# Kernel tuning notes

Hardware: AMD Instinct MI355X
Metric: run time of the kernel (lower is better)

Reference implementation:

```python
import jax, jax.numpy as jnp
import numpy as np
from jax import lax

B, SEQ, C, H, W, OUT, K = 64, 32, 16, 128, 256, 10, 2  # batch, timestamps, channels, hidden, width, classes, substeps/interval


def setup_inputs() -> dict:
    key = jax.random.key(0)
    ks = jax.random.split(key, 16)
    p = lambda k, shape, fan_in: (jax.random.normal(k, shape, dtype=jnp.float32) / np.sqrt(fan_in))
    coeff = lambda k: jax.random.normal(k, (B, SEQ - 1, C), dtype=jnp.float32)
    return {
        'ts': jnp.arange(SEQ, dtype=jnp.float32),
        'coeff_d': coeff(ks[0]), 'coeff_c': coeff(ks[1]), 'coeff_b': coeff(ks[2]), 'coeff_a': coeff(ks[3]),
        # initial MLP: in_size -> width -> width -> hidden (relu)
        'iw0': p(ks[4], (W, C), C), 'ib0': jnp.zeros((W,), jnp.float32),
        'iw1': p(ks[5], (W, W), W), 'ib1': jnp.zeros((W,), jnp.float32),
        'iw2': p(ks[6], (H, W), W), 'ib2': jnp.zeros((H,), jnp.float32),
        # vector-field MLP: hidden -> width -> width -> hidden*in_size (softplus, tanh final)
        'fw0': p(ks[7], (W, H), H), 'fb0': jnp.zeros((W,), jnp.float32),
        'fw1': p(ks[8], (W, W), W), 'fb1': jnp.zeros((W,), jnp.float32),
        'fw2': p(ks[9], (H * C, W), W), 'fb2': jnp.zeros((H * C,), jnp.float32),
        # readout linear: hidden -> out
        'lw': p(ks[10], (OUT, H), H), 'lb': jnp.zeros((OUT,), jnp.float32),
    }


def _forward(ts, coeff_d, coeff_c, coeff_b, coeff_a, iw0, ib0, iw1, ib1, iw2, ib2,
             fw0, fb0, fw1, fb1, fw2, fb2, lw, lb):
    nb, ni, c = coeff_a.shape
    h_dim = iw2.shape[0]

    def init_mlp(x):  # [B,C] -> [B,H]
        h = jax.nn.relu(x @ iw0.T + ib0)
        h = jax.nn.relu(h @ iw1.T + ib1)
        return h @ iw2.T + ib2

    def vf(y):  # [B,H] -> [B,H,C]
        h = jax.nn.softplus(y @ fw0.T + fb0)
        h = jax.nn.softplus(h @ fw1.T + fb1)
        return jnp.tanh(h @ fw2.T + fb2).reshape(nb, h_dim, c)

    def dxdt(frac, i):  # derivative of cubic interpolation on interval i: 3d f^2 + 2c f + b
        return (3.0 * coeff_d[:, i] * frac + 2.0 * coeff_c[:, i]) * frac + coeff_b[:, i]

    def f(frac, i, y):  # ControlTerm.to_ode: dy/dt = vf(y) @ dX/dt
        return jnp.einsum('bhc,bc->bh', vf(y), dxdt(frac, i))

    dts = jnp.diff(ts)
    hsub = dts / K
    idx = jnp.repeat(jnp.arange(ni), K)                                # interval index per substep
    hs = jnp.repeat(hsub, K)                                           # substep size
    fr0 = jnp.tile(jnp.arange(K, dtype=ts.dtype), ni) * hs             # offset within interval at substep start

    def step(y, xs):  # one fixed-size Tsit5 step (Tsitouras 2011 tableau)
        t0, h, i = xs
        k1 = f(t0, i, y)
        k2 = f(t0 + 0.161 * h, i, y + h * (0.161 * k1))
        k3 = f(t0 + 0.327 * h, i, y + h * (-0.008480655492356989 * k1 + 0.335480655492357 * k2))
        k4 = f(t0 + 0.9 * h, i, y + h * (2.8971530571054935 * k1 - 6.359448489975075 * k2 + 4.3622954328695815 * k3))
        k5 = f(t0 + 0.9800255409045097 * h, i, y + h * (5.325864828439257 * k1 - 11.748883564062828 * k2 + 7.4955393428898365 * k3 - 0.09249506636175525 * k4))
        k6 = f(t0 + h, i, y + h * (5.86145544294642 * k1 - 12.92096931784711 * k2 + 8.159367898576159 * k3 - 0.071584973281401 * k4 - 0.028269050394068383 * k5))
        y_new = y + h * (0.09646076681806523 * k1 + 0.01 * k2 + 0.4798896504144996 * k3 + 1.379008574103742 * k4 - 3.290069515436081 * k5 + 2.324710524099774 * k6)
        return y_new, None

    y0 = init_mlp(coeff_a[:, 0])  # X(ts[0]) = a-coefficient at frac=0
    yT, _ = lax.scan(step, y0, (fr0, hs, idx))
    return jax.nn.log_softmax(yT @ lw.T + lb, axis=-1)  # out_size != 1 -> log_softmax


def reference(ts, coeff_d, coeff_c, coeff_b, coeff_a, iw0, ib0, iw1, ib1, iw2, ib2,
              fw0, fb0, fw1, fb1, fw2, fb2, lw, lb):
    return _forward(ts, coeff_d, coeff_c, coeff_b, coeff_a, iw0, ib0, iw1, ib1, iw2, ib2,
                    fw0, fb0, fw1, fb1, fw2, fb2, lw, lb)
```

## Files before the change

### kernel.cpp

```cpp
#include <hip/hip_runtime.h>

#define NBATCH 64
#define NSEQ   32
#define NI     31
#define NC     16
#define NH     128
#define NW     256
#define NOUT   10
#define NSUB   62

#define NGRP 8
#define GB   8
#define NSL  32
#define NBLK (NGRP*NSL)
#define BS   512

#define L1R 8
#define L2R 8
#define L3H 4
#define L3R 64

#define P128 132
#define P256 260

#define WS_BAR   0
#define WS_H1    16384
#define WS_H2    (16384 + 65536)
#define WS_KV    (16384 + 131072)

typedef float f4v __attribute__((ext_vector_type(4)));

__device__ const float ATAB[6][5] = {
  {0.f, 0.f, 0.f, 0.f, 0.f},
  {0.161f, 0.f, 0.f, 0.f, 0.f},
  {-0.008480655492356989f, 0.335480655492357f, 0.f, 0.f, 0.f},
  {2.8971530571054935f, -6.359448489975075f, 4.3622954328695815f, 0.f, 0.f},
  {5.325864828439257f, -11.748883564062828f, 7.4955393428898365f, -0.09249506636175525f, 0.f},
  {5.86145544294642f, -12.92096931784711f, 8.159367898576159f, -0.071584973281401f, -0.028269050394068383f}
};
__device__ const float CNODE[6] = {0.f, 0.161f, 0.327f, 0.9f, 0.9800255409045097f, 1.f};
__device__ const float BTAB[6]  = {0.09646076681806523f, 0.01f, 0.4798896504144996f,
                                   1.379008574103742f, -3.290069515436081f, 2.324710524099774f};

__device__ __forceinline__ float softplusf_(float x) {
  return fmaxf(x, 0.0f) + log1pf(expf(-fabsf(x)));
}
__device__ __forceinline__ float dot4(float4 a, float4 b) {
  return (a.x*b.x + a.y*b.y) + (a.z*b.z + a.w*b.w);
}

__device__ __forceinline__ void sta_f32(float* p, float v) {
  __hip_atomic_store(p, v, __ATOMIC_RELAXED, __HIP_MEMORY_SCOPE_AGENT);
}
__device__ __forceinline__ void sta_f32x4(float* p, f4v v) {
  asm volatile("global_store_dwordx4 %0, %1, off sc0 sc1" :: "v"(p), "v"(v) : "memory");
}
__device__ __forceinline__ f4v lda_f32x4(const float* p) {
  f4v r;
  asm volatile("global_load_dwordx4 %0, %1, off sc0 sc1\n\ts_waitcnt vmcnt(0)"
               : "=v"(r) : "v"(p) : "memory");
  return r;
}

#define SLOT_STRIDE 16
__device__ __forceinline__ void group_barrier(unsigned* slots, int myslot, unsigned seq) {
  asm volatile("s_waitcnt vmcnt(0)" ::: "memory");
  __syncthreads();
  if (threadIdx.x == 0) {
    __hip_atomic_store(&slots[myslot * SLOT_STRIDE], seq,
                       __ATOMIC_RELAXED, __HIP_MEMORY_SCOPE_AGENT);
  }
  if (threadIdx.x < 64) {
    const int lane = threadIdx.x & 31;
    for (;;) {
      const unsigned v = __hip_atomic_load(&slots[lane * SLOT_STRIDE],
                                           __ATOMIC_RELAXED, __HIP_MEMORY_SCOPE_AGENT);
      if (__all(v >= seq)) break;
      __builtin_amdgcn_s_sleep(1);
    }
  }
  __syncthreads();
}

__global__ void bar_init(unsigned* bar) {
  const int n = NGRP * NSL * SLOT_STRIDE;
  for (int i = threadIdx.x; i < n; i += blockDim.x)
    __hip_atomic_store(&bar[i], 0u, __ATOMIC_RELAXED, __HIP_MEMORY_SCOPE_AGENT);
}

__global__ __launch_bounds__(BS) void ncde_fwd(
    const float* __restrict__ ts,
    const float* __restrict__ cd, const float* __restrict__ cc,
    const float* __restrict__ cb, const float* __restrict__ ca,
    const float* __restrict__ iw0, const float* __restrict__ ib0,
    const float* __restrict__ iw1, const float* __restrict__ ib1,
    const float* __restrict__ iw2, const float* __restrict__ ib2,
    const float* __restrict__ fw0, const float* __restrict__ fb0,
    const float* __restrict__ fw1, const float* __restrict__ fb1,
    const float* __restrict__ fw2, const float* __restrict__ fb2,
    const float* __restrict__ lw,  const float* __restrict__ lb,
    unsigned* __restrict__ bar, float* __restrict__ h1c, float* __restrict__ h2c,
    float* __restrict__ kvc, float* __restrict__ out)
{
  const int t   = threadIdx.x;
  const int g   = blockIdx.x & 7;
  const int s   = blockIdx.x >> 3;
  const int gr0 = g * GB;
  unsigned* slots = bar + g * NSL * SLOT_STRIDE;
  unsigned  bseq  = 0;
  float* h1cg = h1c + g * (NSL*GB*L1R);
  float* h2cg = h2c + g * (NSL*GB*L2R);
  float* kvcg = kvc + g * (6*NSL*GB*4);

  __shared__ float fw0s[L1R][P128];
  __shared__ float fw1s[L2R][P256];
  __shared__ float fw2s[L3R][P256];
  __shared__ float h1s[GB][P256];
  __shared__ float h2s[GB][P256];
  __shared__ float ysv[GB][P128];
  __shared__ float yloc[GB][NH];
  __shared__ float dxs[GB][NC];
  __shared__ float x0s[GB][NC];
  __shared__ float fb0s[L1R], fb1s[L2R], fb2s[L3R];
  __shared__ float tss[NSEQ];
  __shared__ float lgs[GB][NOUT], lses[GB];

  {
    if (t < 256) {
      int row = t >> 5, j = t & 31;
      *(float4*)&fw0s[row][4*j] = *(const float4*)&fw0[(size_t)(s*L1R + row)*NH + 4*j];
    }
    {
      int r2 = t >> 6, j2 = t & 63;
      *(float4*)&fw1s[r2][4*j2] = *(const float4*)&fw1[(size_t)(s*L2R + r2)*NW + 4*j2];
    }
    #pragma unroll
    for (int i = 0; i < 8; ++i) {
      int e = t + BS*i; int r2 = e >> 6, j2 = e & 63;
      *(float4*)&fw2s[r2][4*j2] = *(const float4*)&fw2[(size_t)(s*L3R + r2)*NW + 4*j2];
    }
    if (t < L1R) fb0s[t] = fb0[s*L1R + t];
    if (t < L2R) fb1s[t] = fb1[s*L2R + t];
    if (t < L3R) fb2s[t] = fb2[s*L3R + t];
    if (t < NSEQ) tss[t] = ts[t];
  }

  if (t < GB*NC) { int r = t >> 4, c = t & 15; x0s[r][c] = ca[((size_t)(gr0 + r)*NI)*NC + c]; }
  __syncthreads();
  #pragma unroll
  for (int i = 0; i < 4; ++i) {
    int e = t + BS*i; int r = e >> 8, row = e & 255;
    float a = ib0[row];
    #pragma unroll
    for (int k = 0; k < NC; ++k) a += iw0[row*NC + k] * x0s[r][k];
    h1s[r][row] = fmaxf(a, 0.f);
  }
  __syncthreads();
  #pragma unroll
  for (int i = 0; i < 4; ++i) {
    int e = t + BS*i; int r = e >> 8, row = e & 255;
    float a = ib1[row];
    const float4* wr = (const float4*)&iw1[(size_t)row*NW];
    for (int k = 0; k < 64; ++k) a += dot4(wr[k], *(const float4*)&h1s[r][4*k]);
    h2s[r][row] = fmaxf(a, 0.f);
  }
  __syncthreads();
  #pragma unroll
  for (int i = 0; i < 2; ++i) {
    int e = t + BS*i; int r = e >> 7, row = e & 127;
    float a = ib2[row];
    const float4* wr = (const float4*)&iw2[(size_t)row*NW];
    for (int k = 0; k < 64; ++k) a += dot4(wr[k], *(const float4*)&h2s[r][4*k]);
    yloc[r][row] = a;
  }
  __syncthreads();

  const int lane = t & 63;
  const int w    = t >> 6;
  const int yr   = t >> 5, yc4 = 4*(t & 31);
  const int o    = t >> 3, q8 = t & 7;
  const int orow = o & 7, obat = o >> 3;
  const int l3row = t & 63, l3c = t & 15, l3b = t >> 6;

  float4 yreg; f4v kreg[6];
  if (t < 256) yreg = *(const float4*)&yloc[yr][yc4];

  for (int ss = 0; ss < NSUB; ++ss) {
    const int iv = ss >> 1, jv = ss & 1;
    const float h = (tss[iv+1] - tss[iv]) * 0.5f;
    const float t0f = (float)jv * h;

    float cdv = 0.f, ccv = 0.f, cbv = 0.f;
    if (t >= 256 && t < 256 + GB*NC) {
      const int tc = t - 256;
      const size_t base = ((size_t)(gr0 + (tc >> 4))*NI + iv)*NC + (tc & 15);
      cdv = cd[base]; ccv = cc[base]; cbv = cb[base];
    }

    for (int st = 0; st < 6; ++st) {
      if (t < 256) {
        float4 v = yreg;
        for (int jj = 0; jj < st; ++jj) {
          const float a = h * ATAB[st][jj];
          v.x += a*kreg[jj][0]; v.y += a*kreg[jj][1];
          v.z += a*kreg[jj][2]; v.w += a*kreg[jj][3];
        }
        *(float4*)&ysv[yr][yc4] = v;
      } else if (t < 256 + GB*NC) {
        const int tc = t - 256;
        const float f = t0f + CNODE[st] * h;
        dxs[tc >> 4][tc & 15] = (3.f*cdv*f + 2.f*ccv)*f + cbv;
      }
      __syncthreads();

      {
        float a0 = 0.f, a1 = 0.f;
        #pragma unroll
        for (int i = 0; i < 4; i += 2) {
          a0 += dot4(*(const float4*)&fw0s[orow][4*(q8+8*i)],     *(const float4*)&ysv[obat][4*(q8+8*i)]);
          a1 += dot4(*(const float4*)&fw0s[orow][4*(q8+8*(i+1))], *(const float4*)&ysv[obat][4*(q8+8*(i+1))]);
        }
        float a = a0 + a1;
        a += __shfl_xor(a, 1); a += __shfl_xor(a, 2); a += __shfl_xor(a, 4);
        const float praw = __shfl(a, (lane & 7) * 8);
        if (lane < 8)
          sta_f32(&h1cg[(s*GB + w)*L1R + lane], softplusf_(fb0s[lane] + praw));
      }
      group_barrier(slots, s, ++bseq);

      {
        const f4v v = lda_f32x4(h1cg + 4*t);
        *(f4v*)&h1s[(t >> 1) & 7][(t >> 4)*8 + 4*(t & 1)] = v;
      }
      __syncthreads();

      {
        float a0 = 0.f, a1 = 0.f;
        #pragma unroll
        for (int i = 0; i < 8; i += 2) {
          a0 += dot4(*(const float4*)&fw1s[orow][4*(q8+8*i)],     *(const float4*)&h1s[obat][4*(q8+8*i)]);
          a1 += dot4(*(const float4*)&fw1s[orow][4*(q8+8*(i+1))], *(const float4*)&h1s[obat][4*(q8+8*(i+1))]);
        }
        float a = a0 + a1;
        a += __shfl_xor(a, 1); a += __shfl_xor(a, 2); a += __shfl_xor(a, 4);
        const float praw = __shfl(a, (lane & 7) * 8);
        if (lane < 8)
          sta_f32(&h2cg[(s*GB + w)*L2R + lane], softplusf_(fb1s[lane] + praw));
      }
      group_barrier(slots, s, ++bseq);

      {
        const f4v v = lda_f32x4(h2cg + 4*t);
        *(f4v*)&h2s[(t >> 1) & 7][(t >> 4)*8 + 4*(t & 1)] = v;
      }
      __syncthreads();

      {
        const float4* wr = (const float4*)&fw2s[l3row][0];
        const float4* xr = (const float4*)&h2s[l3b][0];
        float a0 = 0.f, a1 = 0.f, a2 = 0.f, a3 = 0.f;
        #pragma unroll 4
        for (int i = 0; i < 64; i += 4) {
          a0 += dot4(wr[i+0], xr[i+0]);
          a1 += dot4(wr[i+1], xr[i+1]);
          a2 += dot4(wr[i+2], xr[i+2]);
          a3 += dot4(wr[i+3], xr[i+3]);
        }
        float v0 = tanhf(((a0+a1)+(a2+a3)) + fb2s[l3row]) * dxs[l3b][l3c];
        v0 += __shfl_xor(v0, 1);
        v0 += __shfl_xor(v0, 2);
        v0 += __shfl_xor(v0, 4);
        v0 += __shfl_xor(v0, 8);
        f4v pk;
        pk[0] = __shfl(v0, 0);  pk[1] = __shfl(v0, 16);
        pk[2] = __shfl(v0, 32); pk[3] = __shfl(v0, 48);
        if (lane == 0)
          sta_f32x4(&kvcg[((st*NSL + s)*GB + w)*4], pk);
      }
      group_barrier(slots, s, ++bseq);

      if (t < 256) {
        kreg[st] = lda_f32x4(kvcg + ((st*NSL + (t & 31))*GB + yr)*4);
      }
    }

    if (t < 256) {
      #pragma unroll
      for (int s2 = 0; s2 < 6; ++s2) {
        const float a = h * BTAB[s2];
        yreg.x += a*kreg[s2][0]; yreg.y += a*kreg[s2][1];
        yreg.z += a*kreg[s2][2]; yreg.w += a*kreg[s2][3];
      }
    }
  }

  if (t < 256) *(float4*)&yloc[yr][yc4] = yreg;
  __syncthreads();

  if (s == 0) {
    if (t < GB*NOUT) {
      const int r = t / NOUT, oo = t % NOUT;
      float a = lb[oo];
      const float4* wr = (const float4*)&lw[(size_t)oo*NH];
      #pragma unroll
      for (int k = 0; k < 32; ++k) a += dot4(wr[k], *(const float4*)&yloc[r][4*k]);
      lgs[r][oo] = a;
    }
    __syncthreads();
    if (t < GB) {
      float m = lgs[t][0];
      for (int oo = 1; oo < NOUT; ++oo) m = fmaxf(m, lgs[t][oo]);
      float se = 0.f;
      for (int oo = 0; oo < NOUT; ++oo) se += expf(lgs[t][oo] - m);
      lses[t] = m + logf(se);
    }
    __syncthreads();
    if (t < GB*NOUT) {
      const int r = t / NOUT, oo = t % NOUT;
      out[(gr0 + r)*NOUT + oo] = lgs[r][oo] - lses[r];
    }
  }
}

extern "C" void kernel_launch(void* const* d_in, const int* in_sizes, int n_in,
                              void* d_out, int out_size, void* d_ws, size_t ws_size,
                              hipStream_t stream) {
  const float* ts  = (const float*)d_in[0];
  const float* cd  = (const float*)d_in[1];
  const float* cc  = (const float*)d_in[2];
  const float* cb  = (const float*)d_in[3];
  const float* ca  = (const float*)d_in[4];
  const float* iw0 = (const float*)d_in[5];
  const float* ib0 = (const float*)d_in[6];
  const float* iw1 = (const float*)d_in[7];
  const float* ib1 = (const float*)d_in[8];
  const float* iw2 = (const float*)d_in[9];
  const float* ib2 = (const float*)d_in[10];
  const float* fw0 = (const float*)d_in[11];
  const float* fb0 = (const float*)d_in[12];
  const float* fw1 = (const float*)d_in[13];
  const float* fb1 = (const float*)d_in[14];
  const float* fw2 = (const float*)d_in[15];
  const float* fb2 = (const float*)d_in[16];
  const float* lw  = (const float*)d_in[17];
  const float* lb  = (const float*)d_in[18];

  char* ws = (char*)d_ws;
  unsigned* bar = (unsigned*)(ws + WS_BAR);
  float* h1c = (float*)(ws + WS_H1);
  float* h2c = (float*)(ws + WS_H2);
  float* kvc = (float*)(ws + WS_KV);

  bar_init<<<1, 512, 0, stream>>>(bar);
  ncde_fwd<<<NBLK, BS, 0, stream>>>(ts, cd, cc, cb, ca, iw0, ib0, iw1, ib1, iw2, ib2,
                                    fw0, fb0, fw1, fb1, fw2, fb2, lw, lb,
                                    bar, h1c, h2c, kvc, (float*)d_out);
}
```

Before: 4.266 ms.

## Map barrier groups to XCCs and use cached loads with acquire fences

Each block reads its hardware XCC id and takes a rank from a per-XCC atomic counter, so every 32-block barrier group sits on one XCC and its sync traffic stays in that XCC's L2. The sc0/sc1 system-coherent loads and stores are replaced by plain accesses plus agent-scope acquire fences. The last barrier of each stage is split into arrive and wait, so only the 256 threads that read k values spin. Correctness now depends on each XCC receiving exactly 32 blocks, which the hardware does not guarantee, and the new spin-loop guard can exit silently on timeout.

```diff
diff --git a/kernel.cpp b/kernel.cpp
--- a/kernel.cpp
+++ b/kernel.cpp
@@ -24,11 +24,12 @@
 #define P256 260
 
 #define WS_BAR   0
-#define WS_H1    16384
-#define WS_H2    (16384 + 65536)
-#define WS_KV    (16384 + 131072)
-
-typedef float f4v __attribute__((ext_vector_type(4)));
+#define WS_CTRL  16384
+#define WS_H1    (16384 + 4096)
+#define WS_H2    (WS_H1 + 65536)
+#define WS_KV    (WS_H2 + 65536)
+
+typedef unsigned long long u64;
 
 __device__ const float ATAB[6][5] = {
   {0.f, 0.f, 0.f, 0.f, 0.f},
@@ -49,43 +50,42 @@
   return (a.x*b.x + a.y*b.y) + (a.z*b.z + a.w*b.w);
 }
 
-__device__ __forceinline__ void sta_f32(float* p, float v) {
-  __hip_atomic_store(p, v, __ATOMIC_RELAXED, __HIP_MEMORY_SCOPE_AGENT);
-}
-__device__ __forceinline__ void sta_f32x4(float* p, f4v v) {
-  asm volatile("global_store_dwordx4 %0, %1, off sc0 sc1" :: "v"(p), "v"(v) : "memory");
-}
-__device__ __forceinline__ f4v lda_f32x4(const float* p) {
-  f4v r;
-  asm volatile("global_load_dwordx4 %0, %1, off sc0 sc1\n\ts_waitcnt vmcnt(0)"
-               : "=v"(r) : "v"(p) : "memory");
-  return r;
+__device__ __forceinline__ void acquire_fence() {
+  __builtin_amdgcn_fence(__ATOMIC_ACQUIRE, "agent");
 }
 
 #define SLOT_STRIDE 16
-__device__ __forceinline__ void group_barrier(unsigned* slots, int myslot, unsigned seq) {
+__device__ __forceinline__ void bar_arrive(unsigned* slots, int myslot, unsigned seq) {
   asm volatile("s_waitcnt vmcnt(0)" ::: "memory");
   __syncthreads();
   if (threadIdx.x == 0) {
     __hip_atomic_store(&slots[myslot * SLOT_STRIDE], seq,
                        __ATOMIC_RELAXED, __HIP_MEMORY_SCOPE_AGENT);
   }
-  if (threadIdx.x < 64) {
-    const int lane = threadIdx.x & 31;
-    for (;;) {
-      const unsigned v = __hip_atomic_load(&slots[lane * SLOT_STRIDE],
-                                           __ATOMIC_RELAXED, __HIP_MEMORY_SCOPE_AGENT);
-      if (__all(v >= seq)) break;
-      __builtin_amdgcn_s_sleep(1);
-    }
-  }
-  __syncthreads();
-}
-
-__global__ void bar_init(unsigned* bar) {
+}
+__device__ __forceinline__ void bar_wait(unsigned* slots, unsigned seq) {
+  const int sl = threadIdx.x & 31;
+  int guard = 0;
+  for (;;) {
+    const unsigned v = __hip_atomic_load(&slots[sl * SLOT_STRIDE],
+                                         __ATOMIC_RELAXED, __HIP_MEMORY_SCOPE_AGENT);
+    if (__all(v >= seq)) break;
+    if (++guard > (1 << 22)) break;
+    __builtin_amdgcn_s_sleep(1);
+  }
+}
+__device__ __forceinline__ void group_barrier(unsigned* slots, int myslot, unsigned seq) {
+  bar_arrive(slots, myslot, seq);
+  if (threadIdx.x < 64) bar_wait(slots, seq);
+  __syncthreads();
+}
+
+__global__ void ws_init(unsigned* bar, u64* rankctr) {
   const int n = NGRP * NSL * SLOT_STRIDE;
   for (int i = threadIdx.x; i < n; i += blockDim.x)
     __hip_atomic_store(&bar[i], 0u, __ATOMIC_RELAXED, __HIP_MEMORY_SCOPE_AGENT);
+  if (threadIdx.x < NGRP)
+    __hip_atomic_store(&rankctr[threadIdx.x], 0ull, __ATOMIC_RELAXED, __HIP_MEMORY_SCOPE_AGENT);
 }
 
 __global__ __launch_bounds__(BS) void ncde_fwd(
@@ -99,12 +99,25 @@
     const float* __restrict__ fw1, const float* __restrict__ fb1,
     const float* __restrict__ fw2, const float* __restrict__ fb2,
     const float* __restrict__ lw,  const float* __restrict__ lb,
-    unsigned* __restrict__ bar, float* __restrict__ h1c, float* __restrict__ h2c,
+    unsigned* __restrict__ bar, u64* __restrict__ rankctr,
+    float* __restrict__ h1c, float* __restrict__ h2c,
     float* __restrict__ kvc, float* __restrict__ out)
 {
-  const int t   = threadIdx.x;
-  const int g   = blockIdx.x & 7;
-  const int s   = blockIdx.x >> 3;
+  const int t = threadIdx.x;
+
+  __shared__ unsigned s_g, s_s;
+  if (t == 0) {
+    unsigned xcc;
+    asm volatile("s_getreg_b32 %0, hwreg(HW_REG_XCC_ID, 0, 32)" : "=s"(xcc));
+    xcc &= 7;
+    u64 r = __hip_atomic_fetch_add(&rankctr[xcc], 1ull,
+                                   __ATOMIC_RELAXED, __HIP_MEMORY_SCOPE_AGENT);
+    s_g = xcc;
+    s_s = (unsigned)r & 31;
+  }
+  __syncthreads();
+  const int g   = s_g;
+  const int s   = s_s;
   const int gr0 = g * GB;
   unsigned* slots = bar + g * NSL * SLOT_STRIDE;
   unsigned  bseq  = 0;
@@ -182,7 +195,7 @@
   const int orow = o & 7, obat = o >> 3;
   const int l3row = t & 63, l3c = t & 15, l3b = t >> 6;
 
-  float4 yreg; f4v kreg[6];
+  float4 yreg, kreg[6];
   if (t < 256) yreg = *(const float4*)&yloc[yr][yc4];
 
   for (int ss = 0; ss < NSUB; ++ss) {
@@ -202,8 +215,8 @@
         float4 v = yreg;
         for (int jj = 0; jj < st; ++jj) {
           const float a = h * ATAB[st][jj];
-          v.x += a*kreg[jj][0]; v.y += a*kreg[jj][1];
-          v.z += a*kreg[jj][2]; v.w += a*kreg[jj][3];
+          v.x += a*kreg[jj].x; v.y += a*kreg[jj].y;
+          v.z += a*kreg[jj].z; v.w += a*kreg[jj].w;
         }
         *(float4*)&ysv[yr][yc4] = v;
       } else if (t < 256 + GB*NC) {
@@ -224,13 +237,14 @@
         a += __shfl_xor(a, 1); a += __shfl_xor(a, 2); a += __shfl_xor(a, 4);
         const float praw = __shfl(a, (lane & 7) * 8);
         if (lane < 8)
-          sta_f32(&h1cg[(s*GB + w)*L1R + lane], softplusf_(fb0s[lane] + praw));
+          h1cg[(s*GB + w)*L1R + lane] = softplusf_(fb0s[lane] + praw);
       }
       group_barrier(slots, s, ++bseq);
-
-      {
-        const f4v v = lda_f32x4(h1cg + 4*t);
-        *(f4v*)&h1s[(t >> 1) & 7][(t >> 4)*8 + 4*(t & 1)] = v;
+      acquire_fence();
+
+      {
+        const float4 v = *(const float4*)(h1cg + 4*t);
+        *(float4*)&h1s[(t >> 1) & 7][(t >> 4)*8 + 4*(t & 1)] = v;
       }
       __syncthreads();
 
@@ -245,13 +259,14 @@
         a += __shfl_xor(a, 1); a += __shfl_xor(a, 2); a += __shfl_xor(a, 4);
         const float praw = __shfl(a, (lane & 7) * 8);
         if (lane < 8)
-          sta_f32(&h2cg[(s*GB + w)*L2R + lane], softplusf_(fb1s[lane] + praw));
+          h2cg[(s*GB + w)*L2R + lane] = softplusf_(fb1s[lane] + praw);
       }
       group_barrier(slots, s, ++bseq);
-
-      {
-        const f4v v = lda_f32x4(h2cg + 4*t);
-        *(f4v*)&h2s[(t >> 1) & 7][(t >> 4)*8 + 4*(t & 1)] = v;
+      acquire_fence();
+
+      {
+        const float4 v = *(const float4*)(h2cg + 4*t);
+        *(float4*)&h2s[(t >> 1) & 7][(t >> 4)*8 + 4*(t & 1)] = v;
       }
       __syncthreads();
 
@@ -271,16 +286,17 @@
         v0 += __shfl_xor(v0, 2);
         v0 += __shfl_xor(v0, 4);
         v0 += __shfl_xor(v0, 8);
-        f4v pk;
-        pk[0] = __shfl(v0, 0);  pk[1] = __shfl(v0, 16);
-        pk[2] = __shfl(v0, 32); pk[3] = __shfl(v0, 48);
+        float4 pk;
+        pk.x = __shfl(v0, 0);  pk.y = __shfl(v0, 16);
+        pk.z = __shfl(v0, 32); pk.w = __shfl(v0, 48);
         if (lane == 0)
-          sta_f32x4(&kvcg[((st*NSL + s)*GB + w)*4], pk);
-      }
-      group_barrier(slots, s, ++bseq);
-
+          *(float4*)&kvcg[((st*NSL + s)*GB + w)*4] = pk;
+      }
+      bar_arrive(slots, s, ++bseq);
       if (t < 256) {
-        kreg[st] = lda_f32x4(kvcg + ((st*NSL + (t & 31))*GB + yr)*4);
+        bar_wait(slots, bseq);
+        acquire_fence();
+        kreg[st] = *(const float4*)(kvcg + ((st*NSL + (t & 31))*GB + yr)*4);
       }
     }
 
@@ -288,8 +304,8 @@
       #pragma unroll
       for (int s2 = 0; s2 < 6; ++s2) {
         const float a = h * BTAB[s2];
-        yreg.x += a*kreg[s2][0]; yreg.y += a*kreg[s2][1];
-        yreg.z += a*kreg[s2][2]; yreg.w += a*kreg[s2][3];
+        yreg.x += a*kreg[s2].x; yreg.y += a*kreg[s2].y;
+        yreg.z += a*kreg[s2].z; yreg.w += a*kreg[s2].w;
       }
     }
   }
@@ -346,13 +362,14 @@
   const float* lb  = (const float*)d_in[18];
 
   char* ws = (char*)d_ws;
-  unsigned* bar = (unsigned*)(ws + WS_BAR);
-  float* h1c = (float*)(ws + WS_H1);
-  float* h2c = (float*)(ws + WS_H2);
-  float* kvc = (float*)(ws + WS_KV);
-
-  bar_init<<<1, 512, 0, stream>>>(bar);
+  unsigned* bar  = (unsigned*)(ws + WS_BAR);
+  u64*      rctr = (u64*)(ws + WS_CTRL);
+  float*    h1c  = (float*)(ws + WS_H1);
+  float*    h2c  = (float*)(ws + WS_H2);
+  float*    kvc  = (float*)(ws + WS_KV);
+
+  ws_init<<<1, 512, 0, stream>>>(bar, rctr);
   ncde_fwd<<<NBLK, BS, 0, stream>>>(ts, cd, cc, cb, ca, iw0, ib0, iw1, ib1, iw2, ib2,
                                     fw0, fb0, fw1, fb1, fw2, fb2, lw, lb,
-                                    bar, h1c, h2c, kvc, (float*)d_out);
-}
+                                    bar, rctr, h1c, h2c, kvc, (float*)d_out);
+}
```

New measurement: 16.92 ms. 297% more time.

## Split batch group into two halves with separate barriers to overlap compute and sync

Applied to the files above, without the earlier changes.

Each 8-row batch group is split into two 4-row halves, each with its own cross-block slot barrier. Arrive and wait are decoupled so one half's layer computation can run while the other half's barrier is pending. The RK stage vectors move from registers into a shared kvs buffer, and the final-layer reduction now goes through shared memory instead of wave shuffles. The cost is twice as many barrier arrivals and extra __syncthreads per stage, plus a spin guard that exits the wait after a fixed count, which could let a slow block read stale data.

```diff
diff --git a/kernel.cpp b/kernel.cpp
--- a/kernel.cpp
+++ b/kernel.cpp
@@ -11,6 +11,7 @@
 
 #define NGRP 8
 #define GB   8
+#define HB   4
 #define NSL  32
 #define NBLK (NGRP*NSL)
 #define BS   512
@@ -24,9 +25,9 @@
 #define P256 260
 
 #define WS_BAR   0
-#define WS_H1    16384
-#define WS_H2    (16384 + 65536)
-#define WS_KV    (16384 + 131072)
+#define WS_H1    32768
+#define WS_H2    (32768 + 65536)
+#define WS_KV    (32768 + 131072)
 
 typedef float f4v __attribute__((ext_vector_type(4)));
 
@@ -52,9 +53,6 @@
 __device__ __forceinline__ void sta_f32(float* p, float v) {
   __hip_atomic_store(p, v, __ATOMIC_RELAXED, __HIP_MEMORY_SCOPE_AGENT);
 }
-__device__ __forceinline__ void sta_f32x4(float* p, f4v v) {
-  asm volatile("global_store_dwordx4 %0, %1, off sc0 sc1" :: "v"(p), "v"(v) : "memory");
-}
 __device__ __forceinline__ f4v lda_f32x4(const float* p) {
   f4v r;
   asm volatile("global_load_dwordx4 %0, %1, off sc0 sc1\n\ts_waitcnt vmcnt(0)"
@@ -63,27 +61,30 @@
 }
 
 #define SLOT_STRIDE 16
-__device__ __forceinline__ void group_barrier(unsigned* slots, int myslot, unsigned seq) {
+__device__ __forceinline__ void bar_arrive(unsigned* slots, int myslot, unsigned seq) {
   asm volatile("s_waitcnt vmcnt(0)" ::: "memory");
   __syncthreads();
   if (threadIdx.x == 0) {
     __hip_atomic_store(&slots[myslot * SLOT_STRIDE], seq,
                        __ATOMIC_RELAXED, __HIP_MEMORY_SCOPE_AGENT);
   }
+}
+__device__ __forceinline__ void bar_wait(unsigned* slots, unsigned seq) {
   if (threadIdx.x < 64) {
-    const int lane = threadIdx.x & 31;
+    const int sl = threadIdx.x & 31;
+    int guard = 0;
     for (;;) {
-      const unsigned v = __hip_atomic_load(&slots[lane * SLOT_STRIDE],
+      const unsigned v = __hip_atomic_load(&slots[sl * SLOT_STRIDE],
                                            __ATOMIC_RELAXED, __HIP_MEMORY_SCOPE_AGENT);
       if (__all(v >= seq)) break;
+      if (++guard > (1 << 22)) break;
       __builtin_amdgcn_s_sleep(1);
     }
   }
-  __syncthreads();
 }
 
 __global__ void bar_init(unsigned* bar) {
-  const int n = NGRP * NSL * SLOT_STRIDE;
+  const int n = NGRP * 2 * NSL * SLOT_STRIDE;
   for (int i = threadIdx.x; i < n; i += blockDim.x)
     __hip_atomic_store(&bar[i], 0u, __ATOMIC_RELAXED, __HIP_MEMORY_SCOPE_AGENT);
 }
@@ -106,11 +107,12 @@
   const int g   = blockIdx.x & 7;
   const int s   = blockIdx.x >> 3;
   const int gr0 = g * GB;
-  unsigned* slots = bar + g * NSL * SLOT_STRIDE;
-  unsigned  bseq  = 0;
-  float* h1cg = h1c + g * (NSL*GB*L1R);
-  float* h2cg = h2c + g * (NSL*GB*L2R);
-  float* kvcg = kvc + g * (6*NSL*GB*4);
+  unsigned* slotsA = bar + (g*2    ) * NSL * SLOT_STRIDE;
+  unsigned* slotsB = bar + (g*2 + 1) * NSL * SLOT_STRIDE;
+  unsigned  seqA = 0, seqB = 0;
+  float* h1cg = h1c + g * (GB*NSL*L1R);
+  float* h2cg = h2c + g * (GB*NSL*L2R);
+  float* kvcg = kvc + g * (6*GB*NSL*4);
 
   __shared__ float fw0s[L1R][P128];
   __shared__ float fw1s[L2R][P256];
@@ -119,8 +121,10 @@
   __shared__ float h2s[GB][P256];
   __shared__ float ysv[GB][P128];
   __shared__ float yloc[GB][NH];
+  __shared__ float kvs[6][GB][NH];
   __shared__ float dxs[GB][NC];
   __shared__ float x0s[GB][NC];
+  __shared__ float kpart[256];
   __shared__ float fb0s[L1R], fb1s[L2R], fb2s[L3R];
   __shared__ float tss[NSEQ];
   __shared__ float lgs[GB][NOUT], lses[GB];
@@ -175,127 +179,156 @@
   }
   __syncthreads();
 
-  const int lane = t & 63;
-  const int w    = t >> 6;
-  const int yr   = t >> 5, yc4 = 4*(t & 31);
-  const int o    = t >> 3, q8 = t & 7;
-  const int orow = o & 7, obat = o >> 3;
-  const int l3row = t & 63, l3c = t & 15, l3b = t >> 6;
-
-  float4 yreg; f4v kreg[6];
-  if (t < 256) yreg = *(const float4*)&yloc[yr][yc4];
-
   for (int ss = 0; ss < NSUB; ++ss) {
     const int iv = ss >> 1, jv = ss & 1;
     const float h = (tss[iv+1] - tss[iv]) * 0.5f;
     const float t0f = (float)jv * h;
 
     float cdv = 0.f, ccv = 0.f, cbv = 0.f;
-    if (t >= 256 && t < 256 + GB*NC) {
-      const int tc = t - 256;
-      const size_t base = ((size_t)(gr0 + (tc >> 4))*NI + iv)*NC + (tc & 15);
+    if (t < 128) {
+      const int tc = t & 63;
+      const size_t base = ((size_t)(gr0 + (t >> 6)*HB + (tc >> 4))*NI + iv)*NC + (tc & 15);
       cdv = cd[base]; ccv = cc[base]; cbv = cb[base];
     }
 
     for (int st = 0; st < 6; ++st) {
+
+      #define PHASE1(hb)                                                          \
+      {                                                                           \
+        {                                            \
+          const int b = (hb)*HB + (t >> 7), c = t & 127;                          \
+          float v = yloc[b][c];                                                   \
+          for (int jj = 0; jj < st; ++jj) v += h * ATAB[st][jj] * kvs[jj][b][c];  \
+          ysv[b][c] = v;                                                          \
+        }                                                                         \
+        if ((t >> 6) == (hb) && t < 128) {                                        \
+          const int tc = t & 63;                                                  \
+          const float f = t0f + CNODE[st] * h;                                    \
+          dxs[(hb)*HB + (tc >> 4)][tc & 15] = (3.f*cdv*f + 2.f*ccv)*f + cbv;      \
+        }                                                                         \
+        __syncthreads();                                                          \
+        {                                               \
+          const int outI = t >> 4, q16 = t & 15;                                  \
+          const int orow = outI & 7, b = (hb)*HB + (outI >> 3);                   \
+          float a = dot4(*(const float4*)&fw0s[orow][4*q16],                      \
+                         *(const float4*)&ysv[b][4*q16])                          \
+                  + dot4(*(const float4*)&fw0s[orow][4*(q16+16)],                 \
+                         *(const float4*)&ysv[b][4*(q16+16)]);                    \
+          a += __shfl_xor(a,1); a += __shfl_xor(a,2);                             \
+          a += __shfl_xor(a,4); a += __shfl_xor(a,8);                             \
+          if (q16 == 0)                                                           \
+            sta_f32(&h1cg[(b*NSL + s)*L1R + orow], softplusf_(fb0s[orow] + a));   \
+        }                                                                         \
+      }
+
+      #define PHASE2(hb)                                                          \
+      {                                                                           \
+        const int outI = t >> 4, q16 = t & 15;                                    \
+        const int orow = outI & 7, b = (hb)*HB + (outI >> 3);                     \
+        float a = 0.f;                                                            \
+        _Pragma("unroll")                                                         \
+        for (int i = 0; i < 4; ++i) {                                             \
+          const int j = q16 + 16*i;                                               \
+          a += dot4(*(const float4*)&fw1s[orow][4*j],                             \
+                    *(const float4*)&h1s[b][4*j]);                                \
+        }                                                                         \
+        a += __shfl_xor(a,1); a += __shfl_xor(a,2);                               \
+        a += __shfl_xor(a,4); a += __shfl_xor(a,8);                               \
+        if (q16 == 0)                                                             \
+          sta_f32(&h2cg[(b*NSL + s)*L2R + orow], softplusf_(fb1s[orow] + a));     \
+      }
+
+      #define PHASE3(hb)                                                          \
+      {                                                                           \
+        const int pair = t >> 1, kh = t & 1;                                      \
+        const int row = pair & 63, b = (hb)*HB + (pair >> 6);                     \
+        const float4* wr = (const float4*)&fw2s[row][0];                          \
+        const float4* xr = (const float4*)&h2s[b][0];                             \
+        float a0 = 0.f, a1 = 0.f;                                                 \
+        _Pragma("unroll 4")                                                       \
+        for (int i = kh*32; i < kh*32 + 32; i += 2) {                             \
+          a0 += dot4(wr[i],   xr[i]);                                             \
+          a1 += dot4(wr[i+1], xr[i+1]);                                           \
+        }                                                                         \
+        float acc = a0 + a1;                                                      \
+        acc += __shfl_xor(acc, 1);                                                \
+        if (kh == 0)                                                              \
+          kpart[pair] = tanhf(acc + fb2s[row]) * dxs[b][row & 15];                \
+        __syncthreads();                                                          \
+        if (t < 16) {                                                             \
+          const int b4 = t >> 2, hh = t & 3;                                      \
+          const float* kp = &kpart[b4*64 + hh*16];                                \
+          float s2 = 0.f;                                                         \
+          _Pragma("unroll")                                                       \
+          for (int c = 0; c < 16; ++c) s2 += kp[c];                               \
+          sta_f32(&kvcg[((st*GB + (hb)*HB + b4)*NSL + s)*4 + hh], s2);            \
+        }                                                                         \
+      }
+
+      PHASE1(0); bar_arrive(slotsA, s, ++seqA);
+      PHASE1(1); bar_arrive(slotsB, s, ++seqB);
+
+      bar_wait(slotsA, seqA); __syncthreads();
       if (t < 256) {
-        float4 v = yreg;
-        for (int jj = 0; jj < st; ++jj) {
-          const float a = h * ATAB[st][jj];
-          v.x += a*kreg[jj][0]; v.y += a*kreg[jj][1];
-          v.z += a*kreg[jj][2]; v.w += a*kreg[jj][3];
-        }
-        *(float4*)&ysv[yr][yc4] = v;
-      } else if (t < 256 + GB*NC) {
-        const int tc = t - 256;
-        const float f = t0f + CNODE[st] * h;
-        dxs[tc >> 4][tc & 15] = (3.f*cdv*f + 2.f*ccv)*f + cbv;
-      }
-      __syncthreads();
-
-      {
-        float a0 = 0.f, a1 = 0.f;
-        #pragma unroll
-        for (int i = 0; i < 4; i += 2) {
-          a0 += dot4(*(const float4*)&fw0s[orow][4*(q8+8*i)],     *(const float4*)&ysv[obat][4*(q8+8*i)]);
-          a1 += dot4(*(const float4*)&fw0s[orow][4*(q8+8*(i+1))], *(const float4*)&ysv[obat][4*(q8+8*(i+1))]);
-        }
-        float a = a0 + a1;
-        a += __shfl_xor(a, 1); a += __shfl_xor(a, 2); a += __shfl_xor(a, 4);
-        const float praw = __shfl(a, (lane & 7) * 8);
-        if (lane < 8)
-          sta_f32(&h1cg[(s*GB + w)*L1R + lane], softplusf_(fb0s[lane] + praw));
-      }
-      group_barrier(slots, s, ++bseq);
-
-      {
         const f4v v = lda_f32x4(h1cg + 4*t);
-        *(f4v*)&h1s[(t >> 1) & 7][(t >> 4)*8 + 4*(t & 1)] = v;
-      }
-      __syncthreads();
-
-      {
-        float a0 = 0.f, a1 = 0.f;
-        #pragma unroll
-        for (int i = 0; i < 8; i += 2) {
-          a0 += dot4(*(const float4*)&fw1s[orow][4*(q8+8*i)],     *(const float4*)&h1s[obat][4*(q8+8*i)]);
-          a1 += dot4(*(const float4*)&fw1s[orow][4*(q8+8*(i+1))], *(const float4*)&h1s[obat][4*(q8+8*(i+1))]);
-        }
-        float a = a0 + a1;
-        a += __shfl_xor(a, 1); a += __shfl_xor(a, 2); a += __shfl_xor(a, 4);
-        const float praw = __shfl(a, (lane & 7) * 8);
-        if (lane < 8)
-          sta_f32(&h2cg[(s*GB + w)*L2R + lane], softplusf_(fb1s[lane] + praw));
-      }
-      group_barrier(slots, s, ++bseq);
-
-      {
+        *(f4v*)&h1s[t >> 6][4*t & 255] = v;
+      }
+      __syncthreads();
+      PHASE2(0); bar_arrive(slotsA, s, ++seqA);
+
+      bar_wait(slotsB, seqB); __syncthreads();
+      if (t < 256) {
+        const f4v v = lda_f32x4(h1cg + 1024 + 4*t);
+        *(f4v*)&h1s[HB + (t >> 6)][4*t & 255] = v;
+      }
+      __syncthreads();
+      PHASE2(1); bar_arrive(slotsB, s, ++seqB);
+
+      bar_wait(slotsA, seqA); __syncthreads();
+      if (t < 256) {
         const f4v v = lda_f32x4(h2cg + 4*t);
-        *(f4v*)&h2s[(t >> 1) & 7][(t >> 4)*8 + 4*(t & 1)] = v;
-      }
-      __syncthreads();
-
-      {
-        const float4* wr = (const float4*)&fw2s[l3row][0];
-        const float4* xr = (const float4*)&h2s[l3b][0];
-        float a0 = 0.f, a1 = 0.f, a2 = 0.f, a3 = 0.f;
-        #pragma unroll 4
-        for (int i = 0; i < 64; i += 4) {
-          a0 += dot4(wr[i+0], xr[i+0]);
-          a1 += dot4(wr[i+1], xr[i+1]);
-          a2 += dot4(wr[i+2], xr[i+2]);
-          a3 += dot4(wr[i+3], xr[i+3]);
-        }
-        float v0 = tanhf(((a0+a1)+(a2+a3)) + fb2s[l3row]) * dxs[l3b][l3c];
-        v0 += __shfl_xor(v0, 1);
-        v0 += __shfl_xor(v0, 2);
-        v0 += __shfl_xor(v0, 4);
-        v0 += __shfl_xor(v0, 8);
-        f4v pk;
-        pk[0] = __shfl(v0, 0);  pk[1] = __shfl(v0, 16);
-        pk[2] = __shfl(v0, 32); pk[3] = __shfl(v0, 48);
-        if (lane == 0)
-          sta_f32x4(&kvcg[((st*NSL + s)*GB + w)*4], pk);
-      }
-      group_barrier(slots, s, ++bseq);
-
+        *(f4v*)&h2s[t >> 6][4*t & 255] = v;
+      }
+      __syncthreads();
+      PHASE3(0); bar_arrive(slotsA, s, ++seqA);
+
+      bar_wait(slotsB, seqB); __syncthreads();
       if (t < 256) {
-        kreg[st] = lda_f32x4(kvcg + ((st*NSL + (t & 31))*GB + yr)*4);
-      }
-    }
-
-    if (t < 256) {
+        const f4v v = lda_f32x4(h2cg + 1024 + 4*t);
+        *(f4v*)&h2s[HB + (t >> 6)][4*t & 255] = v;
+      }
+      __syncthreads();
+      PHASE3(1); bar_arrive(slotsB, s, ++seqB);
+
+      bar_wait(slotsA, seqA); __syncthreads();
+      if (t < 128) {
+        const int b = t >> 5, sl = t & 31;
+        const f4v v = lda_f32x4(kvcg + ((st*GB + b)*NSL + sl)*4);
+        *(f4v*)&kvs[st][b][4*sl] = v;
+      }
+      bar_wait(slotsB, seqB); __syncthreads();
+      if (t < 128) {
+        const int b = HB + (t >> 5), sl = t & 31;
+        const f4v v = lda_f32x4(kvcg + ((st*GB + b)*NSL + sl)*4);
+        *(f4v*)&kvs[st][b][4*sl] = v;
+      }
+      __syncthreads();
+
+      #undef PHASE1
+      #undef PHASE2
+      #undef PHASE3
+    }
+
+    #pragma unroll
+    for (int i = 0; i < 2; ++i) {
+      const int e = t + BS*i, b = e >> 7, c = e & 127;
+      float v = yloc[b][c];
       #pragma unroll
-      for (int s2 = 0; s2 < 6; ++s2) {
-        const float a = h * BTAB[s2];
-        yreg.x += a*kreg[s2][0]; yreg.y += a*kreg[s2][1];
-        yreg.z += a*kreg[s2][2]; yreg.w += a*kreg[s2][3];
-      }
-    }
-  }
-
-  if (t < 256) *(float4*)&yloc[yr][yc4] = yreg;
-  __syncthreads();
+      for (int j = 0; j < 6; ++j) v += h * BTAB[j] * kvs[j][b][c];
+      yloc[b][c] = v;
+    }
+    __syncthreads();
+  }
 
   if (s == 0) {
     if (t < GB*NOUT) {
@@ -351,7 +384,7 @@
   float* h2c = (float*)(ws + WS_H2);
   float* kvc = (float*)(ws + WS_KV);
 
-  bar_init<<<1, 512, 0, stream>>>(bar);
+  bar_init<<<1, 1024, 0, stream>>>(bar);
   ncde_fwd<<<NBLK, BS, 0, stream>>>(ts, cd, cc, cb, ca, iw0, ib0, iw1, ib1, iw2, ib2,
                                     fw0, fb0, fw1, fb1, fw2, fb2, lw, lb,
                                     bar, h1c, h2c, kvc, (float*)d_out);
```

Measured after the change: 5.463 ms. 1.28x slower.

## Compute first vector-field layer redundantly per block to drop one grid barrier

Applied to the files above, without the earlier changes.

Each block now computes the full first vector-field layer (all 256 rows for its 8 batch rows) from fw0 in global memory, instead of a 1/32 slice exchanged through the workspace. This removes one cross-block group barrier and its global round trip per RK stage. The remaining barriers are split into arrive and wait halves, so only the waves that consume the data spin, and a spin guard is added. The cost is 32x redundant layer-1 FLOPs and fw0 reads from L2 on every stage; the spin guard could silently break synchronisation if a wait ever runs that long.

```diff
diff --git a/kernel.cpp b/kernel.cpp
--- a/kernel.cpp
+++ b/kernel.cpp
@@ -15,7 +15,6 @@
 #define NBLK (NGRP*NSL)
 #define BS   512
 
-#define L1R 8
 #define L2R 8
 #define L3H 4
 #define L3R 64
@@ -24,9 +23,8 @@
 #define P256 260
 
 #define WS_BAR   0
-#define WS_H1    16384
-#define WS_H2    (16384 + 65536)
-#define WS_KV    (16384 + 131072)
+#define WS_H2    16384
+#define WS_KV    (16384 + 65536)
 
 typedef float f4v __attribute__((ext_vector_type(4)));
 
@@ -63,23 +61,24 @@
 }
 
 #define SLOT_STRIDE 16
-__device__ __forceinline__ void group_barrier(unsigned* slots, int myslot, unsigned seq) {
+__device__ __forceinline__ void bar_arrive(unsigned* slots, int myslot, unsigned seq) {
   asm volatile("s_waitcnt vmcnt(0)" ::: "memory");
   __syncthreads();
   if (threadIdx.x == 0) {
     __hip_atomic_store(&slots[myslot * SLOT_STRIDE], seq,
                        __ATOMIC_RELAXED, __HIP_MEMORY_SCOPE_AGENT);
   }
-  if (threadIdx.x < 64) {
-    const int lane = threadIdx.x & 31;
-    for (;;) {
-      const unsigned v = __hip_atomic_load(&slots[lane * SLOT_STRIDE],
-                                           __ATOMIC_RELAXED, __HIP_MEMORY_SCOPE_AGENT);
-      if (__all(v >= seq)) break;
-      __builtin_amdgcn_s_sleep(1);
-    }
-  }
-  __syncthreads();
+}
+__device__ __forceinline__ void bar_wait_wave(unsigned* slots, unsigned seq) {
+  const int sl = threadIdx.x & 31;
+  int guard = 0;
+  for (;;) {
+    const unsigned v = __hip_atomic_load(&slots[sl * SLOT_STRIDE],
+                                         __ATOMIC_RELAXED, __HIP_MEMORY_SCOPE_AGENT);
+    if (__all(v >= seq)) break;
+    if (++guard > (1 << 22)) break;
+    __builtin_amdgcn_s_sleep(1);
+  }
 }
 
 __global__ void bar_init(unsigned* bar) {
@@ -99,7 +98,7 @@
     const float* __restrict__ fw1, const float* __restrict__ fb1,
     const float* __restrict__ fw2, const float* __restrict__ fb2,
     const float* __restrict__ lw,  const float* __restrict__ lb,
-    unsigned* __restrict__ bar, float* __restrict__ h1c, float* __restrict__ h2c,
+    unsigned* __restrict__ bar, float* __restrict__ h2c,
     float* __restrict__ kvc, float* __restrict__ out)
 {
   const int t   = threadIdx.x;
@@ -108,28 +107,23 @@
   const int gr0 = g * GB;
   unsigned* slots = bar + g * NSL * SLOT_STRIDE;
   unsigned  bseq  = 0;
-  float* h1cg = h1c + g * (NSL*GB*L1R);
   float* h2cg = h2c + g * (NSL*GB*L2R);
   float* kvcg = kvc + g * (6*NSL*GB*4);
 
-  __shared__ float fw0s[L1R][P128];
   __shared__ float fw1s[L2R][P256];
   __shared__ float fw2s[L3R][P256];
-  __shared__ float h1s[GB][P256];
-  __shared__ float h2s[GB][P256];
+  __shared__ float h1s[GB][NW];
+  __shared__ float h2s[GB][NW];
   __shared__ float ysv[GB][P128];
-  __shared__ float yloc[GB][NH];
   __shared__ float dxs[GB][NC];
   __shared__ float x0s[GB][NC];
-  __shared__ float fb0s[L1R], fb1s[L2R], fb2s[L3R];
+  __shared__ float fb0s[NW];
+  __shared__ float fb1s[L2R], fb2s[L3R];
   __shared__ float tss[NSEQ];
+  __shared__ float yfin[GB][NH];
   __shared__ float lgs[GB][NOUT], lses[GB];
 
   {
-    if (t < 256) {
-      int row = t >> 5, j = t & 31;
-      *(float4*)&fw0s[row][4*j] = *(const float4*)&fw0[(size_t)(s*L1R + row)*NH + 4*j];
-    }
     {
       int r2 = t >> 6, j2 = t & 63;
       *(float4*)&fw1s[r2][4*j2] = *(const float4*)&fw1[(size_t)(s*L2R + r2)*NW + 4*j2];
@@ -139,7 +133,7 @@
       int e = t + BS*i; int r2 = e >> 6, j2 = e & 63;
       *(float4*)&fw2s[r2][4*j2] = *(const float4*)&fw2[(size_t)(s*L3R + r2)*NW + 4*j2];
     }
-    if (t < L1R) fb0s[t] = fb0[s*L1R + t];
+    if (t < NW)  fb0s[t] = fb0[t];
     if (t < L2R) fb1s[t] = fb1[s*L2R + t];
     if (t < L3R) fb2s[t] = fb2[s*L3R + t];
     if (t < NSEQ) tss[t] = ts[t];
@@ -171,7 +165,7 @@
     float a = ib2[row];
     const float4* wr = (const float4*)&iw2[(size_t)row*NW];
     for (int k = 0; k < 64; ++k) a += dot4(wr[k], *(const float4*)&h2s[r][4*k]);
-    yloc[r][row] = a;
+    yfin[r][row] = a;
   }
   __syncthreads();
 
@@ -181,9 +175,10 @@
   const int o    = t >> 3, q8 = t & 7;
   const int orow = o & 7, obat = o >> 3;
   const int l3row = t & 63, l3c = t & 15, l3b = t >> 6;
+  const int r1   = t & 255, half = t >> 8;
 
   float4 yreg; f4v kreg[6];
-  if (t < 256) yreg = *(const float4*)&yloc[yr][yc4];
+  if (t < 256) yreg = *(const float4*)&yfin[yr][yc4];
 
   for (int ss = 0; ss < NSUB; ++ss) {
     const int iv = ss >> 1, jv = ss & 1;
@@ -214,23 +209,22 @@
       __syncthreads();
 
       {
-        float a0 = 0.f, a1 = 0.f;
-        #pragma unroll
-        for (int i = 0; i < 4; i += 2) {
-          a0 += dot4(*(const float4*)&fw0s[orow][4*(q8+8*i)],     *(const float4*)&ysv[obat][4*(q8+8*i)]);
-          a1 += dot4(*(const float4*)&fw0s[orow][4*(q8+8*(i+1))], *(const float4*)&ysv[obat][4*(q8+8*(i+1))]);
+        const float4* wr = (const float4*)&fw0[(size_t)r1 * NH];
+        const int b0 = half * 4;
+        float a0 = 0.f, a1 = 0.f, a2 = 0.f, a3 = 0.f;
+        #pragma unroll 8
+        for (int k = 0; k < 32; ++k) {
+          const float4 wv = wr[k];
+          a0 += dot4(wv, *(const float4*)&ysv[b0+0][4*k]);
+          a1 += dot4(wv, *(const float4*)&ysv[b0+1][4*k]);
+          a2 += dot4(wv, *(const float4*)&ysv[b0+2][4*k]);
+          a3 += dot4(wv, *(const float4*)&ysv[b0+3][4*k]);
         }
-        float a = a0 + a1;
-        a += __shfl_xor(a, 1); a += __shfl_xor(a, 2); a += __shfl_xor(a, 4);
-        const float praw = __shfl(a, (lane & 7) * 8);
-        if (lane < 8)
-          sta_f32(&h1cg[(s*GB + w)*L1R + lane], softplusf_(fb0s[lane] + praw));
-      }
-      group_barrier(slots, s, ++bseq);
-
-      {
-        const f4v v = lda_f32x4(h1cg + 4*t);
-        *(f4v*)&h1s[(t >> 1) & 7][(t >> 4)*8 + 4*(t & 1)] = v;
+        const float bb = fb0s[r1];
+        h1s[b0+0][r1] = softplusf_(bb + a0);
+        h1s[b0+1][r1] = softplusf_(bb + a1);
+        h1s[b0+2][r1] = softplusf_(bb + a2);
+        h1s[b0+3][r1] = softplusf_(bb + a3);
       }
       __syncthreads();
 
@@ -247,7 +241,9 @@
         if (lane < 8)
           sta_f32(&h2cg[(s*GB + w)*L2R + lane], softplusf_(fb1s[lane] + praw));
       }
-      group_barrier(slots, s, ++bseq);
+      bar_arrive(slots, s, ++bseq);
+      if (t < 64) bar_wait_wave(slots, bseq);
+      __syncthreads();
 
       {
         const f4v v = lda_f32x4(h2cg + 4*t);
@@ -277,9 +273,9 @@
         if (lane == 0)
           sta_f32x4(&kvcg[((st*NSL + s)*GB + w)*4], pk);
       }
-      group_barrier(slots, s, ++bseq);
-
+      bar_arrive(slots, s, ++bseq);
       if (t < 256) {
+        bar_wait_wave(slots, bseq);
         kreg[st] = lda_f32x4(kvcg + ((st*NSL + (t & 31))*GB + yr)*4);
       }
     }
@@ -294,7 +290,7 @@
     }
   }
 
-  if (t < 256) *(float4*)&yloc[yr][yc4] = yreg;
+  if (t < 256) *(float4*)&yfin[yr][yc4] = yreg;
   __syncthreads();
 
   if (s == 0) {
@@ -303,7 +299,7 @@
       float a = lb[oo];
       const float4* wr = (const float4*)&lw[(size_t)oo*NH];
       #pragma unroll
-      for (int k = 0; k < 32; ++k) a += dot4(wr[k], *(const float4*)&yloc[r][4*k]);
+      for (int k = 0; k < 32; ++k) a += dot4(wr[k], *(const float4*)&yfin[r][4*k]);
       lgs[r][oo] = a;
     }
     __syncthreads();
@@ -347,12 +343,11 @@
 
   char* ws = (char*)d_ws;
   unsigned* bar = (unsigned*)(ws + WS_BAR);
-  float* h1c = (float*)(ws + WS_H1);
   float* h2c = (float*)(ws + WS_H2);
   float* kvc = (float*)(ws + WS_KV);
 
   bar_init<<<1, 512, 0, stream>>>(bar);
   ncde_fwd<<<NBLK, BS, 0, stream>>>(ts, cd, cc, cb, ca, iw0, ib0, iw1, ib1, iw2, ib2,
                                     fw0, fb0, fw1, fb1, fw2, fb2, lw, lb,
-                                    bar, h1c, h2c, kvc, (float*)d_out);
-}
+                                    bar, h2c, kvc, (float*)d_out);
+}
```

Result: slower. 6.095 ms (+42.9%).
